# Kernel optimization log

Measured on AMD Instinct MI355X. Metric: run time of the kernel, lower is better.

## Reference

```python
import jax, jax.numpy as jnp
import numpy as np

N = 50000      # nodes
E = 800000     # edges (avg degree 16)
F_IN = 128     # in_channels
F_OUT = 64     # out_channels per head
H = 8          # attn heads
ALPHA = 0.2    # leaky relu slope


def setup_inputs() -> dict:
    key = jax.random.key(0)
    k1, k2, k3, k4, k5 = jax.random.split(key, 5)
    x = jax.random.normal(k1, (N, F_IN), dtype=jnp.float32)
    # guarantee every row appears as a source so rowsum > 0 (avoids NaN div)
    src = jnp.concatenate([jnp.arange(N, dtype=jnp.int32),
                           jax.random.randint(k2, (E - N,), 0, N, dtype=jnp.int32)])
    dst = jax.random.randint(k3, (E,), 0, N, dtype=jnp.int32)
    edge = jnp.stack([src, dst])  # [2, E]
    glorot = (6.0 / (F_IN + F_OUT)) ** 0.5
    W = jax.random.uniform(k4, (H, F_IN, F_OUT), jnp.float32, -glorot, glorot)
    a = jax.random.normal(k5, (H, 2 * F_OUT), dtype=jnp.float32) * 0.05
    return {"x": x, "edge": edge, "W": W, "a": a}


def reference(x, edge, W, a):
    # dropout p=0.6 treated in eval mode (identity); activation=None -> identity
    n = x.shape[0]
    src, dst = edge[0], edge[1]
    # per-head projected features: [H, N, F_OUT]
    h = jnp.einsum('nf,hfo->hno', x, W)
    a_src, a_dst = a[:, :F_OUT], a[:, F_OUT:]
    # edge scores a . cat(h_src, h_dst) decomposed into two node-level dots
    s = (jnp.einsum('hno,ho->hn', h, a_src)[:, src]
         + jnp.einsum('hno,ho->hn', h, a_dst)[:, dst])          # [H, E]
    edge_e = jnp.exp(-jax.nn.leaky_relu(s, ALPHA))               # [H, E]
    seg = lambda v: jax.ops.segment_sum(v, src, num_segments=n)
    rowsum = jax.vmap(seg)(edge_e)                               # [H, N] == spmm(e, ones)
    msg = edge_e[..., None] * h[:, dst, :]                       # [H, E, F_OUT]
    h_prime = jax.vmap(seg)(msg)                                 # [H, N, F_OUT]
    out = h_prime / rowsum[..., None]
    # concat heads: [N, H*F_OUT]
    return jnp.transpose(out, (1, 0, 2)).reshape(n, H * F_OUT)
```

## Files before the change

kernel.cpp:

```cpp
#include <hip/hip_runtime.h>
#include <hip/hip_bf16.h>
#include <math.h>

#define N_NODES 50000
#define N_EDGES 800000
#define FIN 128
#define FOUT 64
#define NH 8
#define ALPHA 0.2f
#define HSTRIDE (NH * FOUT)
#define DCAP 128

#define INIT_BPT_B 64
#define INIT_APERM_B 4
#define INIT_DEG_B 49
#define INIT_B (INIT_BPT_B + INIT_APERM_B + INIT_DEG_B)

#define HIST_B 1563
#define PROJ_B 391

typedef __attribute__((ext_vector_type(8))) short bf16x8;
typedef __attribute__((ext_vector_type(4))) float f32x4;
typedef __attribute__((ext_vector_type(2))) float f32x2;

__device__ __forceinline__ unsigned pack_bf2(float lo, float hi) {
    __hip_bfloat162 b = __float22bfloat162_rn(make_float2(lo, hi));
    return *(unsigned*)&b;
}

__device__ __forceinline__ f32x2 bf2f2(unsigned u) {
    f32x2 r;
    r.x = __int_as_float(u << 16);
    r.y = __int_as_float(u & 0xFFFF0000u);
    return r;
}

__global__ __launch_bounds__(256) void gat_init(const float* __restrict__ W,
                                                const float* __restrict__ a,
                                                unsigned* __restrict__ bpt,
                                                float* __restrict__ aperm,
                                                int* __restrict__ deg) {
    const int b = blockIdx.x;
    const int t = threadIdx.x;

    if (b < INIT_BPT_B) {
        const int gt   = b * 256 + t;
        const int dcol = gt >> 5;
        const int kq   = gt & 31;
        const int head = dcol & 7, col = dcol >> 3;
        const float* wp = W + (size_t)head * (FIN * FOUT) + (size_t)(kq * 4) * FOUT + col;
        uint2 pk;
        pk.x = pack_bf2(wp[0],        wp[FOUT]);
        pk.y = pack_bf2(wp[2 * FOUT], wp[3 * FOUT]);
        *(uint2*)(bpt + (size_t)dcol * (FIN / 2) + kq * 2) = pk;
    } else if (b < INIT_BPT_B + INIT_APERM_B) {
        const int idx  = (b - INIT_BPT_B) * 256 + t;
        const int tab  = idx >> 9;
        const int dcol = idx & 511;
        aperm[idx] = a[(dcol & 7) * (2 * FOUT) + tab * FOUT + (dcol >> 3)];
    } else {
        const int i  = ((b - INIT_BPT_B - INIT_APERM_B) * 256 + t) * 4;
        if (i + 3 < N_NODES) {
            *(int4*)(deg + i) = make_int4(0, 0, 0, 0);
        } else {
#pragma unroll
            for (int u = 0; u < 4; ++u)
                if (i + u < N_NODES) deg[i + u] = 0;
        }
    }
}

__global__ __launch_bounds__(256) void gat_histproj(const int* __restrict__ src,
                                                    const int* __restrict__ dst,
                                                    int* __restrict__ deg,
                                                    int* __restrict__ csr_dst,
                                                    const float* __restrict__ x,
                                                    const unsigned short* __restrict__ bpt,
                                                    const float* __restrict__ aperm,
                                                    unsigned short* __restrict__ h2,
                                                    float* __restrict__ ssrc,
                                                    float* __restrict__ sdst) {
    if (blockIdx.x < HIST_B) {
        const int e = (blockIdx.x * 256 + threadIdx.x) * 2;
        if (e + 1 < N_EDGES) {
            const int2 s2 = *(const int2*)(src + e);
            const int2 d2 = *(const int2*)(dst + e);
            const int r0 = atomicAdd(&deg[s2.x], 1);
            csr_dst[s2.x * DCAP + r0] = d2.x;
            const int r1 = atomicAdd(&deg[s2.y], 1);
            csr_dst[s2.y * DCAP + r1] = d2.y;
        } else if (e < N_EDGES) {
            const int s = src[e];
            const int r = atomicAdd(&deg[s], 1);
            csr_dst[s * DCAP + r] = dst[e];
        }
        return;
    }

    const int lane = threadIdx.x & 63;
    const int wid  = (blockIdx.x - HIST_B) * 4 + (threadIdx.x >> 6);
    const int m0   = wid * 32;
    const int l15  = lane & 15;
    const int g    = lane >> 4;

    bf16x8 xf[2][4];
#pragma unroll
    for (int nh = 0; nh < 2; ++nh) {
        int node = m0 + nh * 16 + l15;
        if (node > N_NODES - 1) node = N_NODES - 1;
        const float* p = x + (size_t)node * FIN + g * 8;
#pragma unroll
        for (int ks = 0; ks < 4; ++ks) {
            const float4 a0 = *(const float4*)(p + ks * 32);
            const float4 a1 = *(const float4*)(p + ks * 32 + 4);
            unsigned* u = (unsigned*)&xf[nh][ks];
            u[0] = pack_bf2(a0.x, a0.y);
            u[1] = pack_bf2(a0.z, a0.w);
            u[2] = pack_bf2(a1.x, a1.y);
            u[3] = pack_bf2(a1.z, a1.w);
        }
    }

    float sc1[2][4], sc2[2][4];
#pragma unroll
    for (int nh = 0; nh < 2; ++nh)
#pragma unroll
        for (int r = 0; r < 4; ++r) { sc1[nh][r] = 0.f; sc2[nh][r] = 0.f; }

    for (int stp = 0; stp < 16; ++stp) {
        const int dc0 = stp * 32;
        f32x4 acc[2][2];
#pragma unroll
        for (int dh = 0; dh < 2; ++dh)
#pragma unroll
            for (int nh = 0; nh < 2; ++nh)
                acc[dh][nh] = (f32x4){0.f, 0.f, 0.f, 0.f};

#pragma unroll
        for (int dh = 0; dh < 2; ++dh) {
            const unsigned short* p = bpt + (size_t)(dc0 + dh * 16 + l15) * FIN + g * 8;
#pragma unroll
            for (int ks = 0; ks < 4; ++ks) {
                const bf16x8 af = *(const bf16x8*)(p + ks * 32);
                acc[dh][0] = __builtin_amdgcn_mfma_f32_16x16x32_bf16(af, xf[0][ks], acc[dh][0], 0, 0, 0);
                acc[dh][1] = __builtin_amdgcn_mfma_f32_16x16x32_bf16(af, xf[1][ks], acc[dh][1], 0, 0, 0);
            }
        }

#pragma unroll
        for (int dh = 0; dh < 2; ++dh) {
            const float4 ap1 = *(const float4*)&aperm[dc0 + dh * 16 + g * 4];
            const float4 ap2 = *(const float4*)&aperm[512 + dc0 + dh * 16 + g * 4];
#pragma unroll
            for (int nh = 0; nh < 2; ++nh) {
                sc1[nh][0] += acc[dh][nh][0] * ap1.x;  sc2[nh][0] += acc[dh][nh][0] * ap2.x;
                sc1[nh][1] += acc[dh][nh][1] * ap1.y;  sc2[nh][1] += acc[dh][nh][1] * ap2.y;
                sc1[nh][2] += acc[dh][nh][2] * ap1.z;  sc2[nh][2] += acc[dh][nh][2] * ap2.z;
                sc1[nh][3] += acc[dh][nh][3] * ap1.w;  sc2[nh][3] += acc[dh][nh][3] * ap2.w;
            }
        }

#pragma unroll
        for (int nh = 0; nh < 2; ++nh) {
            const int node = m0 + nh * 16 + l15;
            if (node < N_NODES) {
#pragma unroll
                for (int dh = 0; dh < 2; ++dh) {
                    const int dc = dc0 + dh * 16 + g * 4;
                    uint2 pk;
                    pk.x = pack_bf2(acc[dh][nh][0], acc[dh][nh][1]);
                    pk.y = pack_bf2(acc[dh][nh][2], acc[dh][nh][3]);
                    *(uint2*)((char*)h2 + ((size_t)node * HSTRIDE + dc) * 2) = pk;
                }
            }
        }
    }

#pragma unroll
    for (int nh = 0; nh < 2; ++nh) {
        const int node = m0 + nh * 16 + l15;
        float4 v1 = make_float4(sc1[nh][0], sc1[nh][1], sc1[nh][2], sc1[nh][3]);
        float4 v2 = make_float4(sc2[nh][0], sc2[nh][1], sc2[nh][2], sc2[nh][3]);
        v1.x += __shfl_xor(v1.x, 32, 64); v1.y += __shfl_xor(v1.y, 32, 64);
        v1.z += __shfl_xor(v1.z, 32, 64); v1.w += __shfl_xor(v1.w, 32, 64);
        v2.x += __shfl_xor(v2.x, 32, 64); v2.y += __shfl_xor(v2.y, 32, 64);
        v2.z += __shfl_xor(v2.z, 32, 64); v2.w += __shfl_xor(v2.w, 32, 64);
        if (node < N_NODES) {
            if (g == 0) { *(float4*)&ssrc[node * 8]     = v1; *(float4*)&sdst[node * 8]     = v2; }
            if (g == 1) { *(float4*)&ssrc[node * 8 + 4] = v1; *(float4*)&sdst[node * 8 + 4] = v2; }
        }
    }
}

#define GAT_LD(KK) (*(const uint4*)(h2b + ((size_t)(unsigned)__builtin_amdgcn_readlane(d, (KK)) << 10) + lofs))

#define GAT_FMA(HV, KK) do {                                                                \
    f32x2 ev;                                                                               \
    ev.x = __int_as_float(__builtin_amdgcn_readlane(__float_as_int(e[0]), (KK)));           \
    ev.y = __int_as_float(__builtin_amdgcn_readlane(__float_as_int(e[1]), (KK)));           \
    acc2[0] += ev * bf2f2((HV).x);                                                          \
    ev.x = __int_as_float(__builtin_amdgcn_readlane(__float_as_int(e[2]), (KK)));           \
    ev.y = __int_as_float(__builtin_amdgcn_readlane(__float_as_int(e[3]), (KK)));           \
    acc2[1] += ev * bf2f2((HV).y);                                                          \
    ev.x = __int_as_float(__builtin_amdgcn_readlane(__float_as_int(e[4]), (KK)));           \
    ev.y = __int_as_float(__builtin_amdgcn_readlane(__float_as_int(e[5]), (KK)));           \
    acc2[2] += ev * bf2f2((HV).z);                                                          \
    ev.x = __int_as_float(__builtin_amdgcn_readlane(__float_as_int(e[6]), (KK)));           \
    ev.y = __int_as_float(__builtin_amdgcn_readlane(__float_as_int(e[7]), (KK)));           \
    acc2[3] += ev * bf2f2((HV).w);                                                          \
} while (0)

__global__ __launch_bounds__(256) void gat_gather(const int* __restrict__ deg,
                                                  const int* __restrict__ csr_dst,
                                                  const __hip_bfloat16* __restrict__ h2,
                                                  const float* __restrict__ ssrc,
                                                  const float* __restrict__ sdst,
                                                  float* __restrict__ out) {
    const int n    = (int)((blockIdx.x * 256 + threadIdx.x) >> 6);
    const int lane = threadIdx.x & 63;
    if (n >= N_NODES) return;

    const int start = n * DCAP;
    const int degn  = deg[n];

    const float4 sa = *(const float4*)(ssrc + n * 8);
    const float4 sb = *(const float4*)(ssrc + n * 8 + 4);
    const float s0[8] = {sa.x, sa.y, sa.z, sa.w, sb.x, sb.y, sb.z, sb.w};

    f32x2 acc2[4];
#pragma unroll
    for (int i = 0; i < 4; ++i) acc2[i] = (f32x2){0.f, 0.f};
    float rs[8] = {0.f, 0.f, 0.f, 0.f, 0.f, 0.f, 0.f, 0.f};
    const unsigned lofs = (unsigned)lane * 16u;
    const char* h2b = (const char*)h2;

    for (int base = 0; base < degn; base += 64) {
        const int j      = base + lane;
        const bool valid = j < degn;
        const int d = valid ? __builtin_nontemporal_load(csr_dst + start + j) : 0;
        float4 qa = make_float4(0.f, 0.f, 0.f, 0.f), qb = qa;
        if (valid) {
            qa = *(const float4*)(sdst + d * 8);
            qb = *(const float4*)(sdst + d * 8 + 4);
        }
        const float q[8] = {qa.x, qa.y, qa.z, qa.w, qb.x, qb.y, qb.z, qb.w};
        float e[8];
#pragma unroll
        for (int i = 0; i < 8; ++i) {
            const float sv = s0[i] + q[i];
            const float lr = sv > 0.f ? sv : ALPHA * sv;
            e[i] = valid ? __expf(-lr) : 0.f;
            rs[i] += e[i];
        }

        const int cnt = min(64, degn - base);
        int k = 0;
        if (cnt >= 8) {
            uint4 q0 = GAT_LD(0), q1 = GAT_LD(1), q2 = GAT_LD(2), q3 = GAT_LD(3);
            for (k = 0; k + 8 <= cnt; k += 4) {
                GAT_FMA(q0, k + 0); q0 = GAT_LD(k + 4);
                GAT_FMA(q1, k + 1); q1 = GAT_LD(k + 5);
                GAT_FMA(q2, k + 2); q2 = GAT_LD(k + 6);
                GAT_FMA(q3, k + 3); q3 = GAT_LD(k + 7);
            }
            GAT_FMA(q0, k + 0);
            GAT_FMA(q1, k + 1);
            GAT_FMA(q2, k + 2);
            GAT_FMA(q3, k + 3);
            k += 4;
        }
        for (; k < cnt; ++k) {
            const uint4 qv = GAT_LD(k);
            GAT_FMA(qv, k);
        }
    }

#pragma unroll
    for (int i = 0; i < 8; ++i)
#pragma unroll
        for (int m = 1; m < 64; m <<= 1) rs[i] += __shfl_xor(rs[i], m, 64);

#pragma unroll
    for (int i = 0; i < 8; ++i) {
        const float av = (i & 1) ? acc2[i >> 1].y : acc2[i >> 1].x;
        __builtin_nontemporal_store(av / rs[i], &out[(size_t)n * HSTRIDE + i * 64 + lane]);
    }
}

extern "C" void kernel_launch(void* const* d_in, const int* in_sizes, int n_in,
                              void* d_out, int out_size, void* d_ws, size_t ws_size,
                              hipStream_t stream) {
    const float* x    = (const float*)d_in[0];
    const int*   edge = (const int*)d_in[1];
    const float* W    = (const float*)d_in[2];
    const float* a    = (const float*)d_in[3];
    float*       out  = (float*)d_out;

    char* ws = (char*)d_ws;
    size_t off = 0;
    unsigned short* h2  = (unsigned short*)(ws + off); off += (size_t)N_NODES * HSTRIDE * 2;
    unsigned short* bpt = (unsigned short*)(ws + off); off += (size_t)HSTRIDE * FIN * 2;
    float* aperm  = (float*)(ws + off); off += (size_t)2 * HSTRIDE * sizeof(float);
    float* ssrc   = (float*)(ws + off); off += (size_t)N_NODES * NH * sizeof(float);
    float* sdst   = (float*)(ws + off); off += (size_t)N_NODES * NH * sizeof(float);
    int*   deg    = (int*)  (ws + off); off += (size_t)N_NODES * sizeof(int);
    int*   csrd   = (int*)  (ws + off); off += (size_t)N_NODES * DCAP * sizeof(int);

    const int* srcv = edge;
    const int* dstv = edge + N_EDGES;

    gat_init    <<<INIT_B, 256, 0, stream>>>(W, a, (unsigned*)bpt, aperm, deg);
    gat_histproj<<<HIST_B + PROJ_B, 256, 0, stream>>>(srcv, dstv, deg, csrd,
                                                      x, bpt, aperm, h2, ssrc, sdst);
    gat_gather  <<<(N_NODES + 3) / 4, 256, 0, stream>>>(deg, csrd, (const __hip_bfloat16*)h2,
                                                        ssrc, sdst, out);
}
```

Baseline: 256.5 us.

## Split fused histogram/projection kernel into separate launches with 4-edge vectorized fill

Result: faster. 232.9 us (-9.2%).

```diff
diff --git a/kernel.cpp b/kernel.cpp
--- a/kernel.cpp
+++ b/kernel.cpp
@@ -15,9 +15,6 @@
 #define INIT_APERM_B 4
 #define INIT_DEG_B 49
 #define INIT_B (INIT_BPT_B + INIT_APERM_B + INIT_DEG_B)
-
-#define HIST_B 1563
-#define PROJ_B 391
 
 typedef __attribute__((ext_vector_type(8))) short bf16x8;
 typedef __attribute__((ext_vector_type(4))) float f32x4;
@@ -70,35 +67,42 @@
     }
 }
 
-__global__ __launch_bounds__(256) void gat_histproj(const int* __restrict__ src,
+__global__ __launch_bounds__(256) void gat_histfill(const int* __restrict__ src,
                                                     const int* __restrict__ dst,
                                                     int* __restrict__ deg,
-                                                    int* __restrict__ csr_dst,
-                                                    const float* __restrict__ x,
-                                                    const unsigned short* __restrict__ bpt,
-                                                    const float* __restrict__ aperm,
-                                                    unsigned short* __restrict__ h2,
-                                                    float* __restrict__ ssrc,
-                                                    float* __restrict__ sdst) {
-    if (blockIdx.x < HIST_B) {
-        const int e = (blockIdx.x * 256 + threadIdx.x) * 2;
-        if (e + 1 < N_EDGES) {
-            const int2 s2 = *(const int2*)(src + e);
-            const int2 d2 = *(const int2*)(dst + e);
-            const int r0 = atomicAdd(&deg[s2.x], 1);
-            csr_dst[s2.x * DCAP + r0] = d2.x;
-            const int r1 = atomicAdd(&deg[s2.y], 1);
-            csr_dst[s2.y * DCAP + r1] = d2.y;
-        } else if (e < N_EDGES) {
-            const int s = src[e];
-            const int r = atomicAdd(&deg[s], 1);
-            csr_dst[s * DCAP + r] = dst[e];
-        }
-        return;
-    }
-
+                                                    int* __restrict__ csr_dst) {
+    const int e = (blockIdx.x * 256 + threadIdx.x) * 4;
+    if (e + 3 < N_EDGES) {
+        const int4 s4 = *(const int4*)(src + e);
+        const int4 d4 = *(const int4*)(dst + e);
+        const int r0 = atomicAdd(&deg[s4.x], 1);
+        const int r1 = atomicAdd(&deg[s4.y], 1);
+        const int r2 = atomicAdd(&deg[s4.z], 1);
+        const int r3 = atomicAdd(&deg[s4.w], 1);
+        csr_dst[s4.x * DCAP + r0] = d4.x;
+        csr_dst[s4.y * DCAP + r1] = d4.y;
+        csr_dst[s4.z * DCAP + r2] = d4.z;
+        csr_dst[s4.w * DCAP + r3] = d4.w;
+    } else {
+        for (int u = 0; u < 4; ++u) {
+            const int ee = e + u;
+            if (ee < N_EDGES) {
+                const int s = src[ee];
+                const int r = atomicAdd(&deg[s], 1);
+                csr_dst[s * DCAP + r] = dst[ee];
+            }
+        }
+    }
+}
+
+__global__ __launch_bounds__(256) void gat_proj(const float* __restrict__ x,
+                                                const unsigned short* __restrict__ bpt,
+                                                const float* __restrict__ aperm,
+                                                unsigned short* __restrict__ h2,
+                                                float* __restrict__ ssrc,
+                                                float* __restrict__ sdst) {
     const int lane = threadIdx.x & 63;
-    const int wid  = (blockIdx.x - HIST_B) * 4 + (threadIdx.x >> 6);
+    const int wid  = blockIdx.x * 4 + (threadIdx.x >> 6);
     const int m0   = wid * 32;
     const int l15  = lane & 15;
     const int g    = lane >> 4;
@@ -310,8 +314,8 @@
     const int* dstv = edge + N_EDGES;
 
     gat_init    <<<INIT_B, 256, 0, stream>>>(W, a, (unsigned*)bpt, aperm, deg);
-    gat_histproj<<<HIST_B + PROJ_B, 256, 0, stream>>>(srcv, dstv, deg, csrd,
-                                                      x, bpt, aperm, h2, ssrc, sdst);
+    gat_histfill<<<(N_EDGES / 4 + 255) / 256, 256, 0, stream>>>(srcv, dstv, deg, csrd);
+    gat_proj    <<<(N_NODES + 127) / 128, 256, 0, stream>>>(x, bpt, aperm, h2, ssrc, sdst);
     gat_gather  <<<(N_NODES + 3) / 4, 256, 0, stream>>>(deg, csrd, (const __hip_bfloat16*)h2,
                                                         ssrc, sdst, out);
 }
```
